# Kernel tuning notes

Measured on AMD Instinct MI355X. Metric: run time of the kernel, lower is better.

The kernel has to match this reference:

```python
import jax, jax.numpy as jnp
import numpy as np

S, N, E = 2048, 8, 512
C = 1024          # tot_classes
G = 32            # num_groups
CG = C // G       # classes_per_group = 32
INTERP_PROB = 1.0
LN_EPS = 1e-5


def setup_inputs() -> dict:
    key = jax.random.key(0)
    ks = jax.random.split(key, 8)
    return {
        "x": jax.random.normal(ks[0], (S, N, E), jnp.float32),
        "W1": jax.random.normal(ks[1], (C, E), jnp.float32) * 0.02,
        "b1": jnp.zeros((C,), jnp.float32),
        "class_offsets": jnp.zeros((C,), jnp.float32),
        "W2": jax.random.normal(ks[2], (E, C), jnp.float32) * 0.02,
        "b2": jnp.zeros((E,), jnp.float32),
        "ln_gamma": jnp.ones((E,), jnp.float32),
        "ln_beta": jnp.zeros((E,), jnp.float32),
        # Gumbel noise for the two categorical draws per group
        "g1": jax.random.gumbel(ks[3], (S, N, G, CG), jnp.float32),
        "g2": jax.random.gumbel(ks[4], (S, N, G, CG), jnp.float32),
        # interpolation weight and interp-decision uniform
        "w_interp": jax.random.uniform(ks[5], (S, N, G), jnp.float32),
        "u_interp": jax.random.uniform(ks[6], (S, N, G), jnp.float32),
    }


def _layer_norm(h, gamma, beta):
    mu = jnp.mean(h, axis=-1, keepdims=True)
    var = jnp.mean(jnp.square(h - mu), axis=-1, keepdims=True)
    return (h - mu) * jax.lax.rsqrt(var + LN_EPS) * gamma + beta


def reference(x, W1, b1, class_offsets, W2, b2, ln_gamma, ln_beta,
              g1, g2, w_interp, u_interp):
    # linear1, *3 scale, + class_offsets (min_prob_ratio > 0 path)
    logits = (jnp.einsum('sne,ce->snc', x, W1) + b1) * 3.0 + class_offsets
    lg = logits.reshape(S, N, G, CG)                      # grouped logits
    soft = jax.nn.softmax(lg, axis=-1)                    # per-group softmax
    softmax_out = soft.reshape(S, N, C)
    # flow_sample with straight_through_scale == 1.0:
    # categorical sample (Gumbel-argmax) of two classes, interpolate with
    # prob interp_prob, straight-through derivatives from the softmax.
    logp = jax.nn.log_softmax(lg, axis=-1)
    oh_i = jax.nn.one_hot(jnp.argmax(logp + g1, axis=-1), CG, dtype=lg.dtype)
    oh_j = jax.nn.one_hot(jnp.argmax(logp + g2, axis=-1), CG, dtype=lg.dtype)
    w = w_interp[..., None]
    interp = w * oh_i + (1.0 - w) * oh_j                  # E[interp] = softmax
    hard = jnp.where((u_interp < INTERP_PROB)[..., None], interp, oh_i)
    sampled = soft + jax.lax.stop_gradient(hard - soft)   # straight-through
    sampled = sampled.reshape(S, N, C)
    # projection back to embedding dim + LayerNorm
    pos = _layer_norm(jnp.einsum('snc,ec->sne', sampled, W2) + b2,
                      ln_gamma, ln_beta)
    # reverse_gradient: identity fwd, negated grad
    rev = 2.0 * jax.lax.stop_gradient(sampled) - sampled
    neg = _layer_norm(jnp.einsum('snc,ec->sne', rev, W2) + b2,
                      ln_gamma, ln_beta)
    return sampled, softmax_out, pos, neg
```

## Files before the change

kernel.cpp:

```cpp
#include <hip/hip_runtime.h>

#define ROWS 16384
#define EDIM 512
#define CDIM 1024

#define OFF_SOFT (16384 * 1024)
#define OFF_POS  (2 * 16384 * 1024)
#define OFF_NEG  (2 * 16384 * 1024 + 16384 * 512)

__global__ void transpose_w2_kernel(const float* __restrict__ in,
                                    float* __restrict__ out) {
  __shared__ float tile[32][33];
  const int bx = blockIdx.x * 32;
  const int by = blockIdx.y * 32;
  const int tx = threadIdx.x;
  const int ty = threadIdx.y;
#pragma unroll
  for (int i = 0; i < 32; i += 8)
    tile[ty + i][tx] = in[(size_t)(by + ty + i) * CDIM + bx + tx];
  __syncthreads();
#pragma unroll
  for (int i = 0; i < 32; i += 8)
    out[(size_t)(bx + ty + i) * EDIM + by + tx] = tile[tx][ty + i];
}

#define BM 128
#define BN 128
#define BK 16
#define TM 8
#define TN 8

__global__ __launch_bounds__(256, 2) void gemm1_kernel(
    const float* __restrict__ A, const float* __restrict__ B,
    const float* __restrict__ bias1, const float* __restrict__ coff,
    float* __restrict__ Cout) {
  constexpr int K = EDIM;
  constexpr int Nc = CDIM;
  __shared__ __align__(16) float As[BK][BM + 4];
  __shared__ __align__(16) float Bs[BK][BN + 4];
  const int bm = blockIdx.y * BM;
  const int bn = blockIdx.x * BN;
  const int tid = threadIdx.x;
  const int tx = tid & 15;
  const int ty = tid >> 4;

  float acc[TM][TN] = {};

  const int lrow = tid >> 2;
  const int lk4 = (tid & 3) << 2;

  for (int k0 = 0; k0 < K; k0 += BK) {
#pragma unroll
    for (int i = 0; i < 2; i++) {
      const int row = lrow + i * 64;
      const float4 va =
          *(const float4*)&A[(size_t)(bm + row) * K + k0 + lk4];
      As[lk4 + 0][row] = va.x;
      As[lk4 + 1][row] = va.y;
      As[lk4 + 2][row] = va.z;
      As[lk4 + 3][row] = va.w;
      const float4 vb =
          *(const float4*)&B[(size_t)(bn + row) * K + k0 + lk4];
      Bs[lk4 + 0][row] = vb.x;
      Bs[lk4 + 1][row] = vb.y;
      Bs[lk4 + 2][row] = vb.z;
      Bs[lk4 + 3][row] = vb.w;
    }
    __syncthreads();
#pragma unroll
    for (int k = 0; k < BK; k++) {
      const float4 a0 = *(const float4*)&As[k][ty * TM];
      const float4 a1 = *(const float4*)&As[k][ty * TM + 4];
      const float4 c0 = *(const float4*)&Bs[k][tx * TN];
      const float4 c1 = *(const float4*)&Bs[k][tx * TN + 4];
      const float a[8] = {a0.x, a0.y, a0.z, a0.w, a1.x, a1.y, a1.z, a1.w};
      const float b[8] = {c0.x, c0.y, c0.z, c0.w, c1.x, c1.y, c1.z, c1.w};
#pragma unroll
      for (int i = 0; i < TM; i++)
#pragma unroll
        for (int j = 0; j < TN; j++)
          acc[i][j] = fmaf(a[i], b[j], acc[i][j]);
    }
    __syncthreads();
  }

#pragma unroll
  for (int i = 0; i < TM; i++) {
    const int row = bm + ty * TM + i;
#pragma unroll
    for (int j4 = 0; j4 < 2; j4++) {
      const int col = bn + tx * TN + j4 * 4;
      const float4 bias4 = *(const float4*)&bias1[col];
      const float4 off4 = *(const float4*)&coff[col];
      float4 o;
      o.x = (acc[i][j4 * 4 + 0] + bias4.x) * 3.0f + off4.x;
      o.y = (acc[i][j4 * 4 + 1] + bias4.y) * 3.0f + off4.y;
      o.z = (acc[i][j4 * 4 + 2] + bias4.z) * 3.0f + off4.z;
      o.w = (acc[i][j4 * 4 + 3] + bias4.w) * 3.0f + off4.w;
      *(float4*)&Cout[(size_t)row * Nc + col] = o;
    }
  }
}

__global__ __launch_bounds__(256, 2) void sample_kernel(
    float* __restrict__ out_sampled, float* __restrict__ soft_io,
    float* __restrict__ out_pos, float* __restrict__ out_neg,
    const float* __restrict__ g1, const float* __restrict__ g2,
    const float* __restrict__ wI, const float* __restrict__ uI,
    const float* __restrict__ W2T, const float* __restrict__ b2,
    const float* __restrict__ gam, const float* __restrict__ bet) {
  const int r = blockIdx.x;
  const int tid = threadIdx.x;
  const int lane = tid & 63;
  const int wv = tid >> 6;
  const int cg = lane & 31;

  __shared__ float s_wa[32], s_wb[32];
  __shared__ int s_ci[32], s_cj[32];
  __shared__ float s_red[4];
  __shared__ float s_red2[4];

  float* lg_row = soft_io + (size_t)r * CDIM;
  float* samp_row = out_sampled + (size_t)r * CDIM;
  const float* g1_row = g1 + (size_t)r * CDIM;
  const float* g2_row = g2 + (size_t)r * CDIM;

#pragma unroll
  for (int it = 0; it < 4; it++) {
    const int c = wv * 256 + it * 64 + lane;
    const int g = c >> 5;
    const float logit = lg_row[c];

    float m = logit;
#pragma unroll
    for (int off = 16; off >= 1; off >>= 1)
      m = fmaxf(m, __shfl_xor(m, off));
    const float e = expf(logit - m);
    float ssum = e;
#pragma unroll
    for (int off = 16; off >= 1; off >>= 1) ssum += __shfl_xor(ssum, off);
    const float soft = e / ssum;
    const float logp = (logit - m) - logf(ssum);

    float bv = logp + g1_row[c];
    int bi = cg;
#pragma unroll
    for (int off = 16; off >= 1; off >>= 1) {
      const float ov = __shfl_xor(bv, off);
      const int oi = __shfl_xor(bi, off);
      if (ov > bv || (ov == bv && oi < bi)) { bv = ov; bi = oi; }
    }
    float cv = logp + g2_row[c];
    int cjx = cg;
#pragma unroll
    for (int off = 16; off >= 1; off >>= 1) {
      const float ov = __shfl_xor(cv, off);
      const int oi = __shfl_xor(cjx, off);
      if (ov > cv || (ov == cv && oi < cjx)) { cv = ov; cjx = oi; }
    }

    const float w = wI[(size_t)r * 32 + g];
    const float u = uI[(size_t)r * 32 + g];
    const float interp =
        (cg == bi ? w : 0.0f) + (cg == cjx ? 1.0f - w : 0.0f);
    const float oh = (cg == bi) ? 1.0f : 0.0f;
    const float hard = (u < 1.0f) ? interp : oh;
    samp_row[c] = soft + (hard - soft);
    lg_row[c] = soft;

    if (cg == 0) {
      const bool take = (u < 1.0f);
      s_wa[g] = take ? w : 1.0f;
      s_wb[g] = take ? (1.0f - w) : 0.0f;
      s_ci[g] = g * 32 + bi;
      s_cj[g] = g * 32 + cjx;
    }
  }
  __syncthreads();

  float ax = 0.0f, ay = 0.0f;
#pragma unroll 4
  for (int g = 0; g < 32; g++) {
    const float2 vi = ((const float2*)(W2T + (size_t)s_ci[g] * EDIM))[tid];
    const float2 vj = ((const float2*)(W2T + (size_t)s_cj[g] * EDIM))[tid];
    const float wa = s_wa[g], wb = s_wb[g];
    ax += wa * vi.x + wb * vj.x;
    ay += wa * vi.y + wb * vj.y;
  }
  const int e0 = tid * 2;
  const float2 b2v = ((const float2*)b2)[tid];
  const float hx = ax + b2v.x;
  const float hy = ay + b2v.y;

  float ss = hx + hy;
#pragma unroll
  for (int off = 32; off >= 1; off >>= 1) ss += __shfl_xor(ss, off);
  if (lane == 0) s_red[wv] = ss;
  __syncthreads();
  const float mu =
      (s_red[0] + s_red[1] + s_red[2] + s_red[3]) * (1.0f / 512.0f);
  const float dx = hx - mu, dy = hy - mu;
  float vv = dx * dx + dy * dy;
#pragma unroll
  for (int off = 32; off >= 1; off >>= 1) vv += __shfl_xor(vv, off);
  if (lane == 0) s_red2[wv] = vv;
  __syncthreads();
  const float var =
      (s_red2[0] + s_red2[1] + s_red2[2] + s_red2[3]) * (1.0f / 512.0f);
  const float rsig = 1.0f / sqrtf(var + 1e-5f);

  const float2 gv = ((const float2*)gam)[tid];
  const float2 bv2 = ((const float2*)bet)[tid];
  float2 o;
  o.x = dx * rsig * gv.x + bv2.x;
  o.y = dy * rsig * gv.y + bv2.y;
  ((float2*)(out_pos + (size_t)r * EDIM))[tid] = o;
  ((float2*)(out_neg + (size_t)r * EDIM))[tid] = o;
}

extern "C" void kernel_launch(void* const* d_in, const int* in_sizes, int n_in,
                              void* d_out, int out_size, void* d_ws,
                              size_t ws_size, hipStream_t stream) {
  const float* x = (const float*)d_in[0];
  const float* W1 = (const float*)d_in[1];
  const float* b1 = (const float*)d_in[2];
  const float* coff = (const float*)d_in[3];
  const float* W2 = (const float*)d_in[4];
  const float* b2 = (const float*)d_in[5];
  const float* gam = (const float*)d_in[6];
  const float* bet = (const float*)d_in[7];
  const float* g1 = (const float*)d_in[8];
  const float* g2 = (const float*)d_in[9];
  const float* wI = (const float*)d_in[10];
  const float* uI = (const float*)d_in[11];

  float* out = (float*)d_out;
  float* out_sampled = out;
  float* soft_io = out + OFF_SOFT;
  float* out_pos = out + OFF_POS;
  float* out_neg = out + OFF_NEG;
  float* W2T = (float*)d_ws;

  hipLaunchKernelGGL(transpose_w2_kernel, dim3(CDIM / 32, EDIM / 32),
                     dim3(32, 8), 0, stream, W2, W2T);
  hipLaunchKernelGGL(gemm1_kernel, dim3(CDIM / BN, ROWS / BM), dim3(256), 0,
                     stream, x, W1, b1, coff, soft_io);
  hipLaunchKernelGGL(sample_kernel, dim3(ROWS), dim3(256), 0, stream,
                     out_sampled, soft_io, out_pos, out_neg, g1, g2, wI, uI,
                     W2T, b2, gam, bet);
}
```

Measured before the change: 669.0 us.

## Fuse grouped softmax and Gumbel sampling into GEMM1 epilogue

Moves the per-group softmax, log-softmax, Gumbel argmax, and interpolation into the GEMM1 epilogue. Each thread holds 8 columns and 4 threads cover one 32-class group, so reductions use two shuffles. Logits are no longer written to global memory and read back, and the selected indices and weights are stored as a compact per-group record in workspace. A separate finish kernel then does the W2 gather and LayerNorm. The cost is extra register pressure and Gumbel loads inside the GEMM kernel, which may reduce occupancy.

```diff
diff --git a/kernel.cpp b/kernel.cpp
--- a/kernel.cpp
+++ b/kernel.cpp
@@ -30,12 +30,14 @@
 #define TM 8
 #define TN 8
 
-__global__ __launch_bounds__(256, 2) void gemm1_kernel(
+__global__ __launch_bounds__(256, 2) void gemm1_fused_kernel(
     const float* __restrict__ A, const float* __restrict__ B,
     const float* __restrict__ bias1, const float* __restrict__ coff,
-    float* __restrict__ Cout) {
+    const float* __restrict__ g1, const float* __restrict__ g2,
+    const float* __restrict__ wI, const float* __restrict__ uI,
+    float* __restrict__ out_samp, float* __restrict__ out_soft,
+    float4* __restrict__ rec) {
   constexpr int K = EDIM;
-  constexpr int Nc = CDIM;
   __shared__ __align__(16) float As[BK][BM + 4];
   __shared__ __align__(16) float Bs[BK][BN + 4];
   const int bm = blockIdx.y * BM;
@@ -53,14 +55,12 @@
 #pragma unroll
     for (int i = 0; i < 2; i++) {
       const int row = lrow + i * 64;
-      const float4 va =
-          *(const float4*)&A[(size_t)(bm + row) * K + k0 + lk4];
+      const float4 va = *(const float4*)&A[(size_t)(bm + row) * K + k0 + lk4];
       As[lk4 + 0][row] = va.x;
       As[lk4 + 1][row] = va.y;
       As[lk4 + 2][row] = va.z;
       As[lk4 + 3][row] = va.w;
-      const float4 vb =
-          *(const float4*)&B[(size_t)(bn + row) * K + k0 + lk4];
+      const float4 vb = *(const float4*)&B[(size_t)(bn + row) * K + k0 + lk4];
       Bs[lk4 + 0][row] = vb.x;
       Bs[lk4 + 1][row] = vb.y;
       Bs[lk4 + 2][row] = vb.z;
@@ -84,97 +84,126 @@
     __syncthreads();
   }
 
+  const int col0 = bn + tx * TN;
+  const int cgbase = (tx & 3) * 8;
+  const int g = (bn >> 5) + (tx >> 2);
+  const float4 bias4a = *(const float4*)&bias1[col0];
+  const float4 bias4b = *(const float4*)&bias1[col0 + 4];
+  const float4 off4a = *(const float4*)&coff[col0];
+  const float4 off4b = *(const float4*)&coff[col0 + 4];
+  const float bb[8] = {bias4a.x, bias4a.y, bias4a.z, bias4a.w,
+                       bias4b.x, bias4b.y, bias4b.z, bias4b.w};
+  const float oo[8] = {off4a.x, off4a.y, off4a.z, off4a.w,
+                       off4b.x, off4b.y, off4b.z, off4b.w};
+
 #pragma unroll
   for (int i = 0; i < TM; i++) {
     const int row = bm + ty * TM + i;
-#pragma unroll
-    for (int j4 = 0; j4 < 2; j4++) {
-      const int col = bn + tx * TN + j4 * 4;
-      const float4 bias4 = *(const float4*)&bias1[col];
-      const float4 off4 = *(const float4*)&coff[col];
-      float4 o;
-      o.x = (acc[i][j4 * 4 + 0] + bias4.x) * 3.0f + off4.x;
-      o.y = (acc[i][j4 * 4 + 1] + bias4.y) * 3.0f + off4.y;
-      o.z = (acc[i][j4 * 4 + 2] + bias4.z) * 3.0f + off4.z;
-      o.w = (acc[i][j4 * 4 + 3] + bias4.w) * 3.0f + off4.w;
-      *(float4*)&Cout[(size_t)row * Nc + col] = o;
-    }
-  }
-}
-
-__global__ __launch_bounds__(256, 2) void sample_kernel(
-    float* __restrict__ out_sampled, float* __restrict__ soft_io,
-    float* __restrict__ out_pos, float* __restrict__ out_neg,
-    const float* __restrict__ g1, const float* __restrict__ g2,
-    const float* __restrict__ wI, const float* __restrict__ uI,
-    const float* __restrict__ W2T, const float* __restrict__ b2,
-    const float* __restrict__ gam, const float* __restrict__ bet) {
+    float lg[8];
+#pragma unroll
+    for (int j = 0; j < 8; j++) lg[j] = (acc[i][j] + bb[j]) * 3.0f + oo[j];
+
+    float m = lg[0];
+#pragma unroll
+    for (int j = 1; j < 8; j++) m = fmaxf(m, lg[j]);
+    m = fmaxf(m, __shfl_xor(m, 1));
+    m = fmaxf(m, __shfl_xor(m, 2));
+
+    float e[8], s = 0.0f;
+#pragma unroll
+    for (int j = 0; j < 8; j++) {
+      e[j] = expf(lg[j] - m);
+      s += e[j];
+    }
+    s += __shfl_xor(s, 1);
+    s += __shfl_xor(s, 2);
+    const float inv = 1.0f / s;
+    const float lse = logf(s);
+
+    const float* g1p = &g1[(size_t)row * CDIM + col0];
+    const float* g2p = &g2[(size_t)row * CDIM + col0];
+    const float4 gA0 = *(const float4*)g1p;
+    const float4 gA1 = *(const float4*)(g1p + 4);
+    const float4 gB0 = *(const float4*)g2p;
+    const float4 gB1 = *(const float4*)(g2p + 4);
+    const float ga[8] = {gA0.x, gA0.y, gA0.z, gA0.w, gA1.x, gA1.y, gA1.z, gA1.w};
+    const float gb[8] = {gB0.x, gB0.y, gB0.z, gB0.w, gB1.x, gB1.y, gB1.z, gB1.w};
+
+    float bv = (lg[0] - m) - lse + ga[0];
+    int bi = cgbase;
+    float cv = (lg[0] - m) - lse + gb[0];
+    int cj = cgbase;
+#pragma unroll
+    for (int j = 1; j < 8; j++) {
+      const float lp = (lg[j] - m) - lse;
+      const float v1 = lp + ga[j];
+      if (v1 > bv) { bv = v1; bi = cgbase + j; }
+      const float v2 = lp + gb[j];
+      if (v2 > cv) { cv = v2; cj = cgbase + j; }
+    }
+#pragma unroll
+    for (int off = 1; off <= 2; off <<= 1) {
+      const float ov = __shfl_xor(bv, off);
+      const int oi = __shfl_xor(bi, off);
+      if (ov > bv || (ov == bv && oi < bi)) { bv = ov; bi = oi; }
+      const float ov2 = __shfl_xor(cv, off);
+      const int oi2 = __shfl_xor(cj, off);
+      if (ov2 > cv || (ov2 == cv && oi2 < cj)) { cv = ov2; cj = oi2; }
+    }
+
+    const float w = wI[(size_t)row * 32 + g];
+    const float u = uI[(size_t)row * 32 + g];
+    const bool take = (u < 1.0f);
+
+    float so[8], sa[8];
+#pragma unroll
+    for (int j = 0; j < 8; j++) {
+      const float soft = e[j] * inv;
+      const int cg = cgbase + j;
+      const float interp =
+          (cg == bi ? w : 0.0f) + (cg == cj ? 1.0f - w : 0.0f);
+      const float oh = (cg == bi) ? 1.0f : 0.0f;
+      const float hard = take ? interp : oh;
+      so[j] = soft;
+      sa[j] = soft + (hard - soft);
+    }
+    float* soft_p = &out_soft[(size_t)row * CDIM + col0];
+    float* samp_p = &out_samp[(size_t)row * CDIM + col0];
+    *(float4*)soft_p = make_float4(so[0], so[1], so[2], so[3]);
+    *(float4*)(soft_p + 4) = make_float4(so[4], so[5], so[6], so[7]);
+    *(float4*)samp_p = make_float4(sa[0], sa[1], sa[2], sa[3]);
+    *(float4*)(samp_p + 4) = make_float4(sa[4], sa[5], sa[6], sa[7]);
+
+    if ((tx & 3) == 0) {
+      const float wa = take ? w : 1.0f;
+      const float wb = take ? (1.0f - w) : 0.0f;
+      rec[(size_t)row * 32 + g] =
+          make_float4(__int_as_float(g * 32 + bi), __int_as_float(g * 32 + cj),
+                      wa, wb);
+    }
+  }
+}
+
+__global__ __launch_bounds__(256, 4) void finish_kernel(
+    const float4* __restrict__ rec, const float* __restrict__ W2T,
+    const float* __restrict__ b2, const float* __restrict__ gam,
+    const float* __restrict__ bet, float* __restrict__ out_pos,
+    float* __restrict__ out_neg) {
   const int r = blockIdx.x;
   const int tid = threadIdx.x;
   const int lane = tid & 63;
   const int wv = tid >> 6;
-  const int cg = lane & 31;
 
   __shared__ float s_wa[32], s_wb[32];
   __shared__ int s_ci[32], s_cj[32];
-  __shared__ float s_red[4];
-  __shared__ float s_red2[4];
-
-  float* lg_row = soft_io + (size_t)r * CDIM;
-  float* samp_row = out_sampled + (size_t)r * CDIM;
-  const float* g1_row = g1 + (size_t)r * CDIM;
-  const float* g2_row = g2 + (size_t)r * CDIM;
-
-#pragma unroll
-  for (int it = 0; it < 4; it++) {
-    const int c = wv * 256 + it * 64 + lane;
-    const int g = c >> 5;
-    const float logit = lg_row[c];
-
-    float m = logit;
-#pragma unroll
-    for (int off = 16; off >= 1; off >>= 1)
-      m = fmaxf(m, __shfl_xor(m, off));
-    const float e = expf(logit - m);
-    float ssum = e;
-#pragma unroll
-    for (int off = 16; off >= 1; off >>= 1) ssum += __shfl_xor(ssum, off);
-    const float soft = e / ssum;
-    const float logp = (logit - m) - logf(ssum);
-
-    float bv = logp + g1_row[c];
-    int bi = cg;
-#pragma unroll
-    for (int off = 16; off >= 1; off >>= 1) {
-      const float ov = __shfl_xor(bv, off);
-      const int oi = __shfl_xor(bi, off);
-      if (ov > bv || (ov == bv && oi < bi)) { bv = ov; bi = oi; }
-    }
-    float cv = logp + g2_row[c];
-    int cjx = cg;
-#pragma unroll
-    for (int off = 16; off >= 1; off >>= 1) {
-      const float ov = __shfl_xor(cv, off);
-      const int oi = __shfl_xor(cjx, off);
-      if (ov > cv || (ov == cv && oi < cjx)) { cv = ov; cjx = oi; }
-    }
-
-    const float w = wI[(size_t)r * 32 + g];
-    const float u = uI[(size_t)r * 32 + g];
-    const float interp =
-        (cg == bi ? w : 0.0f) + (cg == cjx ? 1.0f - w : 0.0f);
-    const float oh = (cg == bi) ? 1.0f : 0.0f;
-    const float hard = (u < 1.0f) ? interp : oh;
-    samp_row[c] = soft + (hard - soft);
-    lg_row[c] = soft;
-
-    if (cg == 0) {
-      const bool take = (u < 1.0f);
-      s_wa[g] = take ? w : 1.0f;
-      s_wb[g] = take ? (1.0f - w) : 0.0f;
-      s_ci[g] = g * 32 + bi;
-      s_cj[g] = g * 32 + cjx;
-    }
+  __shared__ float s_red[4], s_red2[4];
+
+  if (tid < 32) {
+    const float4 f = rec[(size_t)r * 32 + tid];
+    s_ci[tid] = __float_as_int(f.x);
+    s_cj[tid] = __float_as_int(f.y);
+    s_wa[tid] = f.z;
+    s_wb[tid] = f.w;
   }
   __syncthreads();
 
@@ -187,7 +216,6 @@
     ax += wa * vi.x + wb * vj.x;
     ay += wa * vi.y + wb * vj.y;
   }
-  const int e0 = tid * 2;
   const float2 b2v = ((const float2*)b2)[tid];
   const float hx = ax + b2v.x;
   const float hy = ay + b2v.y;
@@ -197,8 +225,7 @@
   for (int off = 32; off >= 1; off >>= 1) ss += __shfl_xor(ss, off);
   if (lane == 0) s_red[wv] = ss;
   __syncthreads();
-  const float mu =
-      (s_red[0] + s_red[1] + s_red[2] + s_red[3]) * (1.0f / 512.0f);
+  const float mu = (s_red[0] + s_red[1] + s_red[2] + s_red[3]) * (1.0f / 512.0f);
   const float dx = hx - mu, dy = hy - mu;
   float vv = dx * dx + dy * dy;
 #pragma unroll
@@ -236,16 +263,18 @@
 
   float* out = (float*)d_out;
   float* out_sampled = out;
-  float* soft_io = out + OFF_SOFT;
+  float* out_soft = out + OFF_SOFT;
   float* out_pos = out + OFF_POS;
   float* out_neg = out + OFF_NEG;
+
   float* W2T = (float*)d_ws;
+  float4* rec = (float4*)((char*)d_ws + (size_t)CDIM * EDIM * 4);
 
   hipLaunchKernelGGL(transpose_w2_kernel, dim3(CDIM / 32, EDIM / 32),
                      dim3(32, 8), 0, stream, W2, W2T);
-  hipLaunchKernelGGL(gemm1_kernel, dim3(CDIM / BN, ROWS / BM), dim3(256), 0,
-                     stream, x, W1, b1, coff, soft_io);
-  hipLaunchKernelGGL(sample_kernel, dim3(ROWS), dim3(256), 0, stream,
-                     out_sampled, soft_io, out_pos, out_neg, g1, g2, wI, uI,
-                     W2T, b2, gam, bet);
-}
+  hipLaunchKernelGGL(gemm1_fused_kernel, dim3(CDIM / BN, ROWS / BM), dim3(256),
+                     0, stream, x, W1, b1, coff, g1, g2, wI, uI, out_sampled,
+                     out_soft, rec);
+  hipLaunchKernelGGL(finish_kernel, dim3(ROWS), dim3(256), 0, stream, rec, W2T,
+                     b2, gam, bet, out_pos, out_neg);
+}
```

After: 638.8 us. 4.5% less time.
